# Kernel tuning notes

Hardware: AMD Instinct MI355X
Metric: run time of the kernel (lower is better)

Reference implementation:

```python
import jax, jax.numpy as jnp
import numpy as np

D, K, RANK = 128, 64, 16

def setup_inputs() -> dict:
    key = jax.random.key(0)
    k1, k2, k3, k4, k5 = jax.random.split(key, 5)
    x1 = jax.random.normal(k1, (8, 16384, D), dtype=jnp.float32)
    x2 = jax.random.normal(k2, (8, 16384, D), dtype=jnp.float32)
    scale = (RANK * D) ** -0.5
    W_lin = jax.random.normal(k3, (K, D), dtype=jnp.float32) * (D ** -0.5)
    P = jax.random.normal(k4, (K, D, RANK), dtype=jnp.float32) * scale
    Q = jax.random.normal(k5, (K, D, RANK), dtype=jnp.float32) * scale
    return {"x1": x1, "x2": x2, "W_lin": W_lin, "P": P, "Q": Q}

def reference(x1, x2, W_lin, P, Q):
    z = x1 - x2                                   # (b,n,d)
    s = x1 + x2                                   # (b,n,d)
    lin = jnp.einsum('bnd,kd->bnk', z, W_lin)     # linear term (no bias)
    zP = jnp.einsum('bnd,kdr->bnkr', z, P)
    sQ = jnp.einsum('bnd,kdr->bnkr', s, Q)
    bili = jnp.sum(zP * sQ, axis=-1)              # (b,n,k)
    return lin + bili
```

## Files before the change

### kernel.cpp

```cpp
#include <hip/hip_runtime.h>
#include <hip/hip_bf16.h>

typedef short v8s __attribute__((ext_vector_type(8)));
typedef float v4f __attribute__((ext_vector_type(4)));

#define DD 128
#define KTOT 64
#define RANK 16

#define WOFF 262144

__device__ __forceinline__ unsigned int pk_bf16_trunc(float a, float b) {
  return __builtin_amdgcn_perm(__builtin_bit_cast(unsigned int, b),
                               __builtin_bit_cast(unsigned int, a),
                               0x07060302u);
}

__device__ __forceinline__ unsigned short bf16_rne(float x) {
  unsigned int u = __builtin_bit_cast(unsigned int, x);
  u += 0x7FFFu + ((u >> 16) & 1u);
  return (unsigned short)(u >> 16);
}

__device__ __forceinline__ void stage16(const unsigned short* g, unsigned short* l) {
  __builtin_amdgcn_global_load_lds(
      (const __attribute__((address_space(1))) void*)g,
      (__attribute__((address_space(3))) void*)l, 16, 0, 0);
}

__global__ __launch_bounds__(256)
void swizzle_weights_kernel(const float* __restrict__ Wl,
                            const float* __restrict__ P,
                            const float* __restrict__ Q,
                            unsigned short* __restrict__ ws) {
  const int tid = blockIdx.x * 256 + threadIdx.x;
  if (tid < 16384) {
    const int kg    = tid >> 11;
    const int local = tid & 2047;
    const int rr    = (tid >> 8) & 7;
    const int kk    = (tid >> 6) & 3;
    const int lane  = tid & 63;
    const int q = lane >> 4, c = lane & 15;
    const int k = kg * 8 + (c & 7);
    const int r = rr * 2 + (c >> 3);
    const int dbase = (kk * 4 + q) * 8;
    const float* Pg = P + ((long)k * DD) * RANK + r;
    const float* Qg = Q + ((long)k * DD) * RANK + r;
    union { v8s v; unsigned short h[8]; } po, qo;
#pragma unroll
    for (int j = 0; j < 8; ++j) {
      po.h[j] = bf16_rne(Pg[(long)(dbase + j) * RANK]);
      qo.h[j] = bf16_rne(Qg[(long)(dbase + j) * RANK]);
    }
    *(v8s*)(ws + (long)kg * 32768 + (long)local * 8)         = po.v;
    *(v8s*)(ws + (long)kg * 32768 + 16384 + (long)local * 8) = qo.v;
  } else if (tid < 16384 + 2048) {
    const int t2   = tid - 16384;
    const int kg   = t2 >> 8;
    const int kk   = (t2 >> 6) & 3;
    const int lane = t2 & 63;
    const int q = lane >> 4, c = lane & 15;
    union { v8s v; unsigned short h[8]; } wo;
#pragma unroll
    for (int j = 0; j < 8; ++j) wo.h[j] = 0;
    if (c < 8) {
      const float* wrow = Wl + (long)(kg * 8 + c) * DD + (kk * 4 + q) * 8;
#pragma unroll
      for (int j = 0; j < 8; ++j) wo.h[j] = bf16_rne(wrow[j]);
    }
    *(v8s*)(ws + WOFF + (long)t2 * 8) = wo.v;
  }
}

__global__ __launch_bounds__(512, 2)
void antisym_bilinear_kernel(const float* __restrict__ x1,
                             const float* __restrict__ x2,
                             const unsigned short* __restrict__ wsw,
                             float* __restrict__ out) {
  __shared__ unsigned short lds[2][32768];

  const int b    = blockIdx.x;
  const int tid  = threadIdx.x;
  const int lane = tid & 63;
  const int wave = tid >> 6;
  const int q    = lane >> 4;
  const int c    = lane & 15;

  const int strip0 = b * 16 + wave * 2;

  {
    const unsigned short* gp = wsw + lane * 8;
#pragma unroll
    for (int i = 0; i < 8; ++i) {
      const int ch = (wave * 8 + i) * 512;
      stage16(gp + ch, &lds[0][0] + ch);
    }
  }

  v8s Zf[2][4], Sf[2][4];
#pragma unroll
  for (int t = 0; t < 2; ++t) {
    const int row = (strip0 + t) * 16 + c;
    const float4* p1 = (const float4*)(x1 + (long)row * DD);
    const float4* p2 = (const float4*)(x2 + (long)row * DD);
#pragma unroll
    for (int kk = 0; kk < 4; ++kk) {
      const int i0 = kk * 8 + q * 2;
      float4 a0 = p1[i0], a1 = p1[i0 + 1];
      float4 b0 = p2[i0], b1 = p2[i0 + 1];
      union { v8s v; unsigned int u[4]; } z, s;
      z.u[0] = pk_bf16_trunc(a0.x - b0.x, a0.y - b0.y);
      z.u[1] = pk_bf16_trunc(a0.z - b0.z, a0.w - b0.w);
      z.u[2] = pk_bf16_trunc(a1.x - b1.x, a1.y - b1.y);
      z.u[3] = pk_bf16_trunc(a1.z - b1.z, a1.w - b1.w);
      s.u[0] = pk_bf16_trunc(a0.x + b0.x, a0.y + b0.y);
      s.u[1] = pk_bf16_trunc(a0.z + b0.z, a0.w + b0.w);
      s.u[2] = pk_bf16_trunc(a1.x + b1.x, a1.y + b1.y);
      s.u[3] = pk_bf16_trunc(a1.z + b1.z, a1.w + b1.w);
      Zf[t][kk] = z.v;
      Sf[t][kk] = s.v;
    }
  }

  __syncthreads();

  for (int kg = 0; kg < 8; ++kg) {
    if (kg < 7) {
      const unsigned short* gp = wsw + (long)(kg + 1) * 32768 + lane * 8;
      unsigned short* lbase = &lds[(kg + 1) & 1][0];
#pragma unroll
      for (int i = 0; i < 8; ++i) {
        const int ch = (wave * 8 + i) * 512;
        stage16(gp + ch, lbase + ch);
      }
    }

    v8s Wf[4];
#pragma unroll
    for (int kk = 0; kk < 4; ++kk)
      Wf[kk] = *(const v8s*)(wsw + WOFF + (((long)(kg * 4 + kk) * 64 + lane) * 8));

    const unsigned short* lp = &lds[kg & 1][0] + lane * 8;

    v4f acc[2];
#pragma unroll
    for (int t = 0; t < 2; ++t) acc[t] = (v4f){0.f, 0.f, 0.f, 0.f};

#pragma unroll
    for (int rr = 0; rr < 8; ++rr) {
      v8s Pf[4], Qf[4];
#pragma unroll
      for (int kk = 0; kk < 4; ++kk) {
        const int o = (rr * 4 + kk) * 512;
        Pf[kk] = *(const v8s*)(lp + o);
        Qf[kk] = *(const v8s*)(lp + 16384 + o);
      }
#pragma unroll
      for (int t = 0; t < 2; ++t) {
        v4f ap = (v4f){0.f, 0.f, 0.f, 0.f};
        v4f aq = (v4f){0.f, 0.f, 0.f, 0.f};
#pragma unroll
        for (int kk = 0; kk < 4; ++kk) {
          ap = __builtin_amdgcn_mfma_f32_16x16x32_bf16(Zf[t][kk], Pf[kk], ap, 0, 0, 0);
          aq = __builtin_amdgcn_mfma_f32_16x16x32_bf16(Sf[t][kk], Qf[kk], aq, 0, 0, 0);
        }
        acc[t] += ap * aq;
      }
    }

#pragma unroll
    for (int t = 0; t < 2; ++t) {
#pragma unroll
      for (int kk = 0; kk < 4; ++kk)
        acc[t] = __builtin_amdgcn_mfma_f32_16x16x32_bf16(Zf[t][kk], Wf[kk], acc[t], 0, 0, 0);
    }

#pragma unroll
    for (int t = 0; t < 2; ++t) {
      float v0 = acc[t][0], v1 = acc[t][1], v2 = acc[t][2], v3 = acc[t][3];
      v0 += __shfl_xor(v0, 8, 64);
      v1 += __shfl_xor(v1, 8, 64);
      v2 += __shfl_xor(v2, 8, 64);
      v3 += __shfl_xor(v3, 8, 64);
      const int row0 = (strip0 + t) * 16 + q * 4;
      const int cc = c & 7;
      float* op = out + (long)row0 * KTOT + kg * 8 + cc;
      if (c < 8) { op[0 * KTOT] = v0; op[1 * KTOT] = v1; }
      else       { op[2 * KTOT] = v2; op[3 * KTOT] = v3; }
    }

    __syncthreads();
  }
}

extern "C" void kernel_launch(void* const* d_in, const int* in_sizes, int n_in,
                              void* d_out, int out_size, void* d_ws, size_t ws_size,
                              hipStream_t stream) {
  (void)in_sizes; (void)n_in; (void)ws_size; (void)out_size;
  const float* x1 = (const float*)d_in[0];
  const float* x2 = (const float*)d_in[1];
  const float* Wl = (const float*)d_in[2];
  const float* P  = (const float*)d_in[3];
  const float* Q  = (const float*)d_in[4];
  float* out = (float*)d_out;
  unsigned short* ws = (unsigned short*)d_ws;

  hipLaunchKernelGGL(swizzle_weights_kernel, dim3(72), dim3(256), 0, stream,
                     Wl, P, Q, ws);
  hipLaunchKernelGGL(antisym_bilinear_kernel, dim3(512), dim3(512), 0, stream,
                     x1, x2, ws, out);
}
```

Baseline: 218.3 us.

## Pipeline weight staging in quarter-size LDS phases with finer double buffering

Reorders the swizzled weight buffer into 8K-element phases, each holding two rank pairs of P and Q, and double-buffers them in a 32 KB LDS array instead of 128 KB. The main loop now prefetches and syncs per quarter k-group, which allows more blocks per CU and shortens the prefetch granularity. It also loads the linear weight fragments just before use and adds s_setprio around the MFMA sections. The cost is four times as many barriers per k-group.

```diff
diff --git a/kernel.cpp b/kernel.cpp
--- a/kernel.cpp
+++ b/kernel.cpp
@@ -36,7 +36,6 @@
   const int tid = blockIdx.x * 256 + threadIdx.x;
   if (tid < 16384) {
     const int kg    = tid >> 11;
-    const int local = tid & 2047;
     const int rr    = (tid >> 8) & 7;
     const int kk    = (tid >> 6) & 3;
     const int lane  = tid & 63;
@@ -52,8 +51,10 @@
       po.h[j] = bf16_rne(Pg[(long)(dbase + j) * RANK]);
       qo.h[j] = bf16_rne(Qg[(long)(dbase + j) * RANK]);
     }
-    *(v8s*)(ws + (long)kg * 32768 + (long)local * 8)         = po.v;
-    *(v8s*)(ws + (long)kg * 32768 + 16384 + (long)local * 8) = qo.v;
+    const long base  = (long)(kg * 4 + (rr >> 1)) * 8192;
+    const long local = (long)(((rr & 1) * 4 + kk) * 64 + lane) * 8;
+    *(v8s*)(ws + base + local)        = po.v;
+    *(v8s*)(ws + base + 4096 + local) = qo.v;
   } else if (tid < 16384 + 2048) {
     const int t2   = tid - 16384;
     const int kg   = t2 >> 8;
@@ -72,12 +73,12 @@
   }
 }
 
-__global__ __launch_bounds__(512, 2)
+__global__ __launch_bounds__(512)
 void antisym_bilinear_kernel(const float* __restrict__ x1,
                              const float* __restrict__ x2,
                              const unsigned short* __restrict__ wsw,
                              float* __restrict__ out) {
-  __shared__ unsigned short lds[2][32768];
+  __shared__ unsigned short lds[2][8192];
 
   const int b    = blockIdx.x;
   const int tid  = threadIdx.x;
@@ -88,13 +89,10 @@
 
   const int strip0 = b * 16 + wave * 2;
 
-  {
-    const unsigned short* gp = wsw + lane * 8;
-#pragma unroll
-    for (int i = 0; i < 8; ++i) {
-      const int ch = (wave * 8 + i) * 512;
-      stage16(gp + ch, &lds[0][0] + ch);
-    }
+#pragma unroll
+  for (int i = 0; i < 2; ++i) {
+    const int ch = (wave * 2 + i) * 512;
+    stage16(wsw + ch + lane * 8, &lds[0][0] + ch);
   }
 
   v8s Zf[2][4], Sf[2][4];
@@ -125,55 +123,61 @@
   __syncthreads();
 
   for (int kg = 0; kg < 8; ++kg) {
-    if (kg < 7) {
-      const unsigned short* gp = wsw + (long)(kg + 1) * 32768 + lane * 8;
-      unsigned short* lbase = &lds[(kg + 1) & 1][0];
-#pragma unroll
-      for (int i = 0; i < 8; ++i) {
-        const int ch = (wave * 8 + i) * 512;
-        stage16(gp + ch, lbase + ch);
+    v4f acc[2];
+#pragma unroll
+    for (int t = 0; t < 2; ++t) acc[t] = (v4f){0.f, 0.f, 0.f, 0.f};
+
+#pragma unroll
+    for (int qq = 0; qq < 4; ++qq) {
+      const int ph = kg * 4 + qq;
+
+      if (qq < 3 || kg < 7) {
+        const unsigned short* gp = wsw + (long)(ph + 1) * 8192 + lane * 8;
+        unsigned short* lb = &lds[(qq + 1) & 1][0];
+#pragma unroll
+        for (int i = 0; i < 2; ++i) {
+          const int ch = (wave * 2 + i) * 512;
+          stage16(gp + ch, lb + ch);
+        }
       }
-    }
-
-    v8s Wf[4];
-#pragma unroll
-    for (int kk = 0; kk < 4; ++kk)
-      Wf[kk] = *(const v8s*)(wsw + WOFF + (((long)(kg * 4 + kk) * 64 + lane) * 8));
-
-    const unsigned short* lp = &lds[kg & 1][0] + lane * 8;
-
-    v4f acc[2];
-#pragma unroll
-    for (int t = 0; t < 2; ++t) acc[t] = (v4f){0.f, 0.f, 0.f, 0.f};
-
-#pragma unroll
-    for (int rr = 0; rr < 8; ++rr) {
-      v8s Pf[4], Qf[4];
-#pragma unroll
-      for (int kk = 0; kk < 4; ++kk) {
-        const int o = (rr * 4 + kk) * 512;
-        Pf[kk] = *(const v8s*)(lp + o);
-        Qf[kk] = *(const v8s*)(lp + 16384 + o);
+
+      const unsigned short* lp = &lds[qq & 1][0] + lane * 8;
+      __builtin_amdgcn_s_setprio(1);
+#pragma unroll
+      for (int rr2 = 0; rr2 < 2; ++rr2) {
+        v8s Pf[4], Qf[4];
+#pragma unroll
+        for (int kk = 0; kk < 4; ++kk) {
+          const int o = (rr2 * 4 + kk) * 512;
+          Pf[kk] = *(const v8s*)(lp + o);
+          Qf[kk] = *(const v8s*)(lp + 4096 + o);
+        }
+#pragma unroll
+        for (int t = 0; t < 2; ++t) {
+          v4f ap = (v4f){0.f, 0.f, 0.f, 0.f};
+          v4f aq = (v4f){0.f, 0.f, 0.f, 0.f};
+#pragma unroll
+          for (int kk = 0; kk < 4; ++kk) {
+            ap = __builtin_amdgcn_mfma_f32_16x16x32_bf16(Zf[t][kk], Pf[kk], ap, 0, 0, 0);
+            aq = __builtin_amdgcn_mfma_f32_16x16x32_bf16(Sf[t][kk], Qf[kk], aq, 0, 0, 0);
+          }
+          acc[t] += ap * aq;
+        }
       }
-#pragma unroll
-      for (int t = 0; t < 2; ++t) {
-        v4f ap = (v4f){0.f, 0.f, 0.f, 0.f};
-        v4f aq = (v4f){0.f, 0.f, 0.f, 0.f};
-#pragma unroll
-        for (int kk = 0; kk < 4; ++kk) {
-          ap = __builtin_amdgcn_mfma_f32_16x16x32_bf16(Zf[t][kk], Pf[kk], ap, 0, 0, 0);
-          aq = __builtin_amdgcn_mfma_f32_16x16x32_bf16(Sf[t][kk], Qf[kk], aq, 0, 0, 0);
-        }
-        acc[t] += ap * aq;
-      }
-    }
-
-#pragma unroll
-    for (int t = 0; t < 2; ++t) {
-#pragma unroll
-      for (int kk = 0; kk < 4; ++kk)
-        acc[t] = __builtin_amdgcn_mfma_f32_16x16x32_bf16(Zf[t][kk], Wf[kk], acc[t], 0, 0, 0);
-    }
+      __builtin_amdgcn_s_setprio(0);
+
+      __syncthreads();
+    }
+
+    __builtin_amdgcn_s_setprio(1);
+#pragma unroll
+    for (int kk = 0; kk < 4; ++kk) {
+      const v8s Wfk = *(const v8s*)(wsw + WOFF + (((long)(kg * 4 + kk) * 64 + lane) * 8));
+#pragma unroll
+      for (int t = 0; t < 2; ++t)
+        acc[t] = __builtin_amdgcn_mfma_f32_16x16x32_bf16(Zf[t][kk], Wfk, acc[t], 0, 0, 0);
+    }
+    __builtin_amdgcn_s_setprio(0);
 
 #pragma unroll
     for (int t = 0; t < 2; ++t) {
@@ -188,8 +192,6 @@
       if (c < 8) { op[0 * KTOT] = v0; op[1 * KTOT] = v1; }
       else       { op[2 * KTOT] = v2; op[3 * KTOT] = v3; }
     }
-
-    __syncthreads();
   }
 }
 
```

Measured after the change: 220.0 us. Within noise of the previous version (+0.8%).
